# Kernel tuning notes

Hardware: AMD Instinct MI355X
Metric: run time of the kernel (lower is better)

## Reference

```python
import jax, jax.numpy as jnp
import numpy as np

F = 39          # total fields = 13 numeric + 26 categorical
NUM_NUM = 13
N_CAT = 26
V = 100000      # vocab per categorical field
E = 16          # embed size
RED = max(1, F // 3)  # SE reduction size = 13
P = F * (F - 1) // 2  # 741 pairs
HID = [1024, 512, 256]
B = 4096

I_IDX, J_IDX = np.triu_indices(F, k=1)  # static pair indices, len P


def setup_inputs() -> dict:
    key = jax.random.key(0)
    ks = jax.random.split(key, 16)
    s = 0.01
    inp = {
        "cat": jax.random.randint(ks[0], (B, N_CAT), 0, V),
        "num": jax.random.normal(ks[1], (B, NUM_NUM), dtype=jnp.float32),
        "embed_tables": jax.random.normal(ks[2], (N_CAT, V, E), dtype=jnp.float32) * s,
        "num_emb": jax.random.normal(ks[3], (NUM_NUM, E), dtype=jnp.float32) * s,
        "W_se1": jax.random.normal(ks[4], (F, RED), dtype=jnp.float32) * 0.1,
        "W_se2": jax.random.normal(ks[5], (RED, F), dtype=jnp.float32) * 0.1,
        "W_bil": jax.random.normal(ks[6], (F, E, E), dtype=jnp.float32) * 0.1,  # per-field Linear(E,E,no bias), [field,in,out]
        "W_d1": jax.random.normal(ks[7], (2 * P * E, HID[0]), dtype=jnp.float32) * 0.01,
        "b_d1": jnp.zeros((HID[0],), dtype=jnp.float32),
        "W_d2": jax.random.normal(ks[8], (HID[0], HID[1]), dtype=jnp.float32) * 0.02,
        "b_d2": jnp.zeros((HID[1],), dtype=jnp.float32),
        "W_d3": jax.random.normal(ks[9], (HID[1], HID[2]), dtype=jnp.float32) * 0.02,
        "b_d3": jnp.zeros((HID[2],), dtype=jnp.float32),
        "W_out": jax.random.normal(ks[10], (HID[2], 1), dtype=jnp.float32) * 0.02,
        "b_out": jnp.zeros((1,), dtype=jnp.float32),
    }
    return inp


def _bilinear_each(x, W_bil):
    # x: [B,F,E]; project each field with its own matrix, then pairwise multiply.
    proj = jnp.einsum("bfe,fed->bfd", x, W_bil)            # [B,F,E]
    return proj[:, I_IDX, :] * x[:, J_IDX, :]               # [B,P,E]


def reference(cat, num, embed_tables, num_emb, W_se1, W_se2, W_bil,
              W_d1, b_d1, W_d2, b_d2, W_d3, b_d3, W_out, b_out):
    # categorical embeddings: per-field gather -> [B, N_CAT, E]
    cat_embed = embed_tables[jnp.arange(N_CAT)[None, :], cat]
    # numerical "embeddings": value * learned vector -> [B, NUM_NUM, E]
    num_embed = num[:, :, None] * num_emb[None, :, :]
    x = jnp.concatenate([num_embed, cat_embed], axis=1)     # [B,F,E]

    # SENET gating
    Z = jnp.mean(x, axis=-1)                                 # [B,F]
    A = jax.nn.relu(jax.nn.relu(Z @ W_se1) @ W_se2)          # [B,F]
    V = x * A[:, :, None]

    se_bi = _bilinear_each(V, W_bil)                         # [B,P,E]
    bi = _bilinear_each(x, W_bil)                            # [B,P,E]
    hid = jnp.concatenate([se_bi, bi], axis=1).reshape(x.shape[0], -1)  # [B, 2*P*E]

    h = jax.nn.relu(hid @ W_d1 + b_d1)
    h = jax.nn.relu(h @ W_d2 + b_d2)
    h = jax.nn.relu(h @ W_d3 + b_d3)
    return h @ W_out + b_out                                 # [B,1]
```

## Files before the change

kernel.cpp:

```cpp
#include <hip/hip_runtime.h>

typedef unsigned short u16;
typedef __attribute__((ext_vector_type(8))) __bf16 bf16x8;
typedef __attribute__((ext_vector_type(4))) float f32x4;

#define NF    39
#define NNUM  13
#define NCAT  26
#define VOC   100000
#define NPAIR 741
#define KHID  23712
#define BATCH 4096
#define HD1   1024
#define HD2   512
#define HD3   256

__device__ __forceinline__ u16 f2bf(float f) {
  unsigned u = __builtin_bit_cast(unsigned, f);
  return (u16)((u + 0x7fffu + ((u >> 16) & 1u)) >> 16);
}

__device__ __forceinline__ void gload16(const void* g, void* l) {
  __builtin_amdgcn_global_load_lds((const __attribute__((address_space(1))) void*)g,
                                   (__attribute__((address_space(3))) void*)l, 16, 0, 0);
}

__global__ __launch_bounds__(256) void fuse_front(
    const int* __restrict__ cat, const float* __restrict__ num,
    const float* __restrict__ tables, const float* __restrict__ nemb,
    const float* __restrict__ Wse1, const float* __restrict__ Wse2,
    const float* __restrict__ Wbil, u16* __restrict__ hid)
{
  __shared__ float xs[NF][16];
  __shared__ float wb[NF][16][16];
  __shared__ float pr[NF][16];
  __shared__ float Zs[NF], Ts[NNUM], As[NF];
  __shared__ unsigned char pis[NPAIR], pjs[NPAIR];

  const int b = blockIdx.x;
  const int tid = threadIdx.x;

  for (int i = tid; i < NF * 256; i += 256) ((float*)wb)[i] = Wbil[i];

  for (int t = tid; t < NNUM * 16; t += 256) {
    int f = t >> 4, e = t & 15;
    xs[f][e] = num[b * NNUM + f] * nemb[t];
  }
  for (int t = tid; t < NCAT * 16; t += 256) {
    int c = t >> 4, e = t & 15;
    int cv = cat[b * NCAT + c];
    xs[NNUM + c][e] = tables[((size_t)c * VOC + cv) * 16 + e];
  }
  for (int p = tid; p < NPAIR; p += 256) {
    int i = 0, rs = 0;
    while (p >= rs + (NF - 1 - i)) { rs += NF - 1 - i; ++i; }
    pis[p] = (unsigned char)i;
    pjs[p] = (unsigned char)(i + 1 + (p - rs));
  }
  __syncthreads();

  if (tid < NF) {
    float s = 0.f;
    #pragma unroll
    for (int e = 0; e < 16; ++e) s += xs[tid][e];
    Zs[tid] = s * (1.f / 16.f);
  }
  __syncthreads();
  if (tid < NNUM) {
    float s = 0.f;
    for (int f = 0; f < NF; ++f) s += Zs[f] * Wse1[f * NNUM + tid];
    Ts[tid] = fmaxf(s, 0.f);
  }
  __syncthreads();
  if (tid < NF) {
    float s = 0.f;
    for (int r = 0; r < NNUM; ++r) s += Ts[r] * Wse2[r * NF + tid];
    As[tid] = fmaxf(s, 0.f);
  }
  for (int t = tid; t < NF * 16; t += 256) {
    int f = t >> 4, d = t & 15;
    float s = 0.f;
    #pragma unroll
    for (int e = 0; e < 16; ++e) s += xs[f][e] * wb[f][e][d];
    pr[f][d] = s;
  }
  __syncthreads();

  u16* hr = hid + (size_t)b * KHID;
  for (int idx = tid; idx < NPAIR * 16; idx += 256) {
    int p = idx >> 4, e = idx & 15;
    int i = pis[p], j = pjs[p];
    float bv = pr[i][e] * xs[j][e];
    hr[NPAIR * 16 + idx] = f2bf(bv);
    hr[idx] = f2bf(As[i] * As[j] * bv);
  }
}

__global__ __launch_bounds__(256) void transpose_cast(
    const float* __restrict__ in, u16* __restrict__ out, int K, int N)
{
  __shared__ float t[32][33];
  const int k0 = blockIdx.x * 32, n0 = blockIdx.y * 32;
  const int c = threadIdx.x & 31, r = threadIdx.x >> 5;
  #pragma unroll
  for (int it = 0; it < 4; ++it)
    t[r + it * 8][c] = in[(size_t)(k0 + r + it * 8) * N + n0 + c];
  __syncthreads();
  #pragma unroll
  for (int it = 0; it < 4; ++it)
    out[(size_t)(n0 + r + it * 8) * K + k0 + c] = f2bf(t[c][r + it * 8]);
}

__global__ __launch_bounds__(512, 2) void gemm8_bf16(
    const u16* __restrict__ A, const u16* __restrict__ Bt,
    float* __restrict__ Cp, int M, int N, int K, int totku, int kpb)
{
  __shared__ __align__(16) u16 lds[4 * 16384];

  const int tid = threadIdx.x;
  const int wid = tid >> 6, lane = tid & 63;

  const int d = blockIdx.x;
  const int x = d & 7;
  const int j = d >> 3;
  const int mb = ((x & 3) << 2) | (j & 3);
  const int nb = (j >> 2) & 3;
  const int sb = ((x >> 2) << 1) | (j >> 4);

  const int ks0 = sb * kpb;
  const int kunits = (totku - ks0 < kpb) ? (totku - ks0) : kpb;

  const int wm = wid >> 2, wn = wid & 3;
  const int lrow = lane & 15, c0 = lane >> 4;

  const int rA = tid >> 2;
  const int csrc = (tid & 3) ^ ((rA >> 1) & 3);
  const u16* pA = A  + (size_t)((size_t)mb * 256 + rA) * K + (size_t)ks0 * 32 + csrc * 8;
  const u16* pB = Bt + (size_t)((size_t)nb * 256 + rA) * K + (size_t)ks0 * 32 + csrc * 8;
  const size_t rowskip = (size_t)128 * K;
  u16* dA = lds + wid * 512;
  u16* dB = lds + 8192 + wid * 512;

  int offA[8], offB[4];
  #pragma unroll
  for (int m = 0; m < 8; ++m) {
    int r = wm * 128 + m * 16 + lrow;
    offA[m] = r * 32 + ((c0 ^ ((r >> 1) & 3)) << 3);
  }
  #pragma unroll
  for (int n = 0; n < 4; ++n) {
    int r = wn * 64 + n * 16 + lrow;
    offB[n] = 8192 + r * 32 + ((c0 ^ ((r >> 1) & 3)) << 3);
  }

  f32x4 acc[8][4];
  #pragma unroll
  for (int m = 0; m < 8; ++m)
    #pragma unroll
    for (int n = 0; n < 4; ++n) acc[m][n] = f32x4{0.f, 0.f, 0.f, 0.f};

  #pragma unroll
  for (int u = 0; u < 3; ++u) {
    const u16* a = pA + u * 32;
    const u16* b = pB + u * 32;
    u16* da = dA + u * 16384;
    u16* db = dB + u * 16384;
    gload16(a, da);            gload16(a + rowskip, da + 4096);
    gload16(b, db);            gload16(b + rowskip, db + 4096);
  }

  for (int t = 0; t < kunits; ++t) {
    asm volatile("s_waitcnt vmcnt(8)" ::: "memory");
    __builtin_amdgcn_s_barrier();
    __builtin_amdgcn_sched_barrier(0);

    {
      int su = (t + 3 < kunits) ? (t + 3) : (kunits - 1);
      const u16* a = pA + (size_t)su * 32;
      const u16* b = pB + (size_t)su * 32;
      int so = ((t + 3) & 3) * 16384;
      u16* da = dA + so;
      u16* db = dB + so;
      gload16(a, da);          gload16(a + rowskip, da + 4096);
      gload16(b, db);          gload16(b + rowskip, db + 4096);
    }

    const u16* sl = lds + (t & 3) * 16384;
    bf16x8 af[8], bg[4];
    #pragma unroll
    for (int m = 0; m < 8; ++m) af[m] = *reinterpret_cast<const bf16x8*>(sl + offA[m]);
    #pragma unroll
    for (int n = 0; n < 4; ++n) bg[n] = *reinterpret_cast<const bf16x8*>(sl + offB[n]);

    __builtin_amdgcn_s_setprio(1);
    #pragma unroll
    for (int m = 0; m < 8; ++m)
      #pragma unroll
      for (int n = 0; n < 4; ++n)
        acc[m][n] = __builtin_amdgcn_mfma_f32_16x16x32_bf16(af[m], bg[n], acc[m][n], 0, 0, 0);
    __builtin_amdgcn_s_setprio(0);

    __builtin_amdgcn_sched_barrier(0);
  }

  float* C = Cp + (size_t)sb * M * N;
  #pragma unroll
  for (int m = 0; m < 8; ++m) {
    const int rb = mb * 256 + wm * 128 + m * 16 + (lane >> 4) * 4;
    #pragma unroll
    for (int n = 0; n < 4; ++n) {
      const int col = nb * 256 + wn * 64 + n * 16 + (lane & 15);
      #pragma unroll
      for (int j2 = 0; j2 < 4; ++j2)
        __builtin_nontemporal_store(acc[m][n][j2], &C[(size_t)(rb + j2) * N + col]);
    }
  }
}

__global__ __launch_bounds__(256) void gemm_bf16(
    const u16* __restrict__ A, const u16* __restrict__ Bt,
    float* __restrict__ Cp, int M, int N, int K, int kps)
{
  __shared__ __align__(16) u16 lA[128 * 32];
  __shared__ __align__(16) u16 lB[128 * 32];
  const int tid = threadIdx.x;
  const int mb = blockIdx.x, nb = blockIdx.y, sb = blockIdx.z;
  const int w = tid >> 6, lane = tid & 63;
  const int wr = (w >> 1) * 64, wc = (w & 1) * 64;
  const int lrow = lane & 15, lko = (lane >> 4) * 8;

  f32x4 acc[4][4];
  #pragma unroll
  for (int m = 0; m < 4; ++m)
    #pragma unroll
    for (int n = 0; n < 4; ++n) acc[m][n] = f32x4{0.f, 0.f, 0.f, 0.f};

  const u16* Ab = A + (size_t)mb * 128 * K;
  const u16* Bb = Bt + (size_t)nb * 128 * K;
  const int r0 = tid >> 2, inn = (tid & 3) * 8;
  const int l0 = (tid & ~63) * 8, l1 = ((256 + tid) & ~63) * 8;

  const int ks1 = (sb + 1) * kps;
  for (int ks = sb * kps; ks < ks1; ++ks) {
    const int k0 = ks * 32;
    __syncthreads();
    gload16(Ab + (size_t)r0 * K + k0 + inn,        lA + l0);
    gload16(Ab + (size_t)(r0 + 64) * K + k0 + inn, lA + l1);
    gload16(Bb + (size_t)r0 * K + k0 + inn,        lB + l0);
    gload16(Bb + (size_t)(r0 + 64) * K + k0 + inn, lB + l1);
    __syncthreads();
    bf16x8 af[4], bg[4];
    #pragma unroll
    for (int m = 0; m < 4; ++m)
      af[m] = *reinterpret_cast<const bf16x8*>(&lA[(wr + m * 16 + lrow) * 32 + lko]);
    #pragma unroll
    for (int n = 0; n < 4; ++n)
      bg[n] = *reinterpret_cast<const bf16x8*>(&lB[(wc + n * 16 + lrow) * 32 + lko]);
    #pragma unroll
    for (int m = 0; m < 4; ++m)
      #pragma unroll
      for (int n = 0; n < 4; ++n)
        acc[m][n] = __builtin_amdgcn_mfma_f32_16x16x32_bf16(af[m], bg[n], acc[m][n], 0, 0, 0);
  }

  float* C = Cp + (size_t)sb * M * N;
  #pragma unroll
  for (int m = 0; m < 4; ++m) {
    const int rb = mb * 128 + wr + m * 16 + (lane >> 4) * 4;
    #pragma unroll
    for (int n = 0; n < 4; ++n) {
      const int col = nb * 128 + wc + n * 16 + (lane & 15);
      #pragma unroll
      for (int j = 0; j < 4; ++j)
        __builtin_nontemporal_store(acc[m][n][j], &C[(size_t)(rb + j) * N + col]);
    }
  }
}

__global__ __launch_bounds__(256) void reduce_bias_relu_bf16(
    const float* __restrict__ part, int S, size_t MN,
    const float* __restrict__ bias, int nmask, u16* __restrict__ out)
{
  for (size_t i = blockIdx.x * 256ull + threadIdx.x; i < MN; i += (size_t)gridDim.x * 256) {
    float s = 0.f;
    for (int k = 0; k < S; ++k) s += __builtin_nontemporal_load(&part[(size_t)k * MN + i]);
    s += bias[i & nmask];
    out[i] = f2bf(fmaxf(s, 0.f));
  }
}

__global__ __launch_bounds__(256) void reduce_bias_relu_f32(
    const float* __restrict__ part, int S, size_t MN,
    const float* __restrict__ bias, int nmask, float* __restrict__ out)
{
  for (size_t i = blockIdx.x * 256ull + threadIdx.x; i < MN; i += (size_t)gridDim.x * 256) {
    float s = 0.f;
    for (int k = 0; k < S; ++k) s += __builtin_nontemporal_load(&part[(size_t)k * MN + i]);
    s += bias[i & nmask];
    out[i] = fmaxf(s, 0.f);
  }
}

__global__ __launch_bounds__(256) void final_dot(
    const float* __restrict__ h3, const float* __restrict__ Wout,
    const float* __restrict__ bout, float* __restrict__ out)
{
  const int row = blockIdx.x * 4 + (threadIdx.x >> 6);
  const int lane = threadIdx.x & 63;
  const float* hr = h3 + (size_t)row * HD3;
  float s = 0.f;
  #pragma unroll
  for (int i = 0; i < 4; ++i) s += hr[lane + i * 64] * Wout[lane + i * 64];
  #pragma unroll
  for (int off = 32; off; off >>= 1) s += __shfl_down(s, off, 64);
  if (lane == 0) out[row] = s + bout[0];
}

extern "C" void kernel_launch(void* const* d_in, const int* in_sizes, int n_in,
                              void* d_out, int out_size, void* d_ws, size_t ws_size,
                              hipStream_t stream)
{
  const int*   cat    = (const int*)  d_in[0];
  const float* num    = (const float*)d_in[1];
  const float* tables = (const float*)d_in[2];
  const float* nemb   = (const float*)d_in[3];
  const float* Wse1   = (const float*)d_in[4];
  const float* Wse2   = (const float*)d_in[5];
  const float* Wbil   = (const float*)d_in[6];
  const float* Wd1    = (const float*)d_in[7];
  const float* bd1    = (const float*)d_in[8];
  const float* Wd2    = (const float*)d_in[9];
  const float* bd2    = (const float*)d_in[10];
  const float* Wd3    = (const float*)d_in[11];
  const float* bd3    = (const float*)d_in[12];
  const float* Wout   = (const float*)d_in[13];
  const float* bout   = (const float*)d_in[14];

  char* ws = (char*)d_ws;
  u16*   hid  = (u16*)  (ws + 0ull);
  u16*   W1t  = (u16*)  (ws + 194248704ull);
  float* part = (float*)(ws + 242810880ull);
  u16*   W2t  = (u16*)  (ws + 309919744ull);
  u16*   W3t  = (u16*)  (ws + 310968320ull);
  u16*   h1b  = (u16*)  (ws + 0ull);
  u16*   h2b  = (u16*)  (ws + 8388608ull);
  float* h3f  = (float*)(ws + 12582912ull);

  transpose_cast<<<dim3(KHID / 32, HD1 / 32), 256, 0, stream>>>(Wd1, W1t, KHID, HD1);
  transpose_cast<<<dim3(HD1 / 32, HD2 / 32), 256, 0, stream>>>(Wd2, W2t, HD1, HD2);
  transpose_cast<<<dim3(HD2 / 32, HD3 / 32), 256, 0, stream>>>(Wd3, W3t, HD2, HD3);
  fuse_front<<<BATCH, 256, 0, stream>>>(cat, num, tables, nemb, Wse1, Wse2, Wbil, hid);

  gemm8_bf16<<<256, 512, 0, stream>>>(hid, W1t, part, BATCH, HD1, KHID, 741, 186);
  reduce_bias_relu_bf16<<<2048, 256, 0, stream>>>(part, 4, (size_t)BATCH * HD1, bd1, HD1 - 1, h1b);

  gemm_bf16<<<dim3(BATCH / 128, HD2 / 128, 2), 256, 0, stream>>>(h1b, W2t, part, BATCH, HD2, HD1, 16);
  reduce_bias_relu_bf16<<<2048, 256, 0, stream>>>(part, 2, (size_t)BATCH * HD2, bd2, HD2 - 1, h2b);

  gemm_bf16<<<dim3(BATCH / 128, HD3 / 128, 4), 256, 0, stream>>>(h2b, W3t, part, BATCH, HD3, HD2, 4);
  reduce_bias_relu_f32<<<2048, 256, 0, stream>>>(part, 4, (size_t)BATCH * HD3, bd3, HD3 - 1, h3f);

  final_dot<<<BATCH / 4, 256, 0, stream>>>(h3f, Wout, bout, (float*)d_out);
}
```

Before: 381.5 us.

## Restructure big GEMM main loop into ping-pong half-tile phases with staggered loads

The first dense-layer GEMM now splits each K unit into two half-phases of 16 MFMAs. Each phase interleaves LDS fragment reads and global-to-LDS prefetches for A and B separately. A and B get their own 4-slot ring buffers, and the loop is unrolled by two K units, with a tail step for an odd count. The aim is to overlap LDS reads, async global loads and MFMA work better and to hold fewer A fragments in registers, at the cost of more barriers per iteration and tricky vmcnt accounting.

After: 365.0 us. 1.05x faster.

```diff
diff --git a/kernel.cpp b/kernel.cpp
--- a/kernel.cpp
+++ b/kernel.cpp
@@ -111,35 +111,33 @@
     out[(size_t)(n0 + r + it * 8) * K + k0 + c] = f2bf(t[c][r + it * 8]);
 }
 
-__global__ __launch_bounds__(512, 2) void gemm8_bf16(
+__global__ __launch_bounds__(512, 2) void gemm8p_bf16(
     const u16* __restrict__ A, const u16* __restrict__ Bt,
     float* __restrict__ Cp, int M, int N, int K, int totku, int kpb)
 {
-  __shared__ __align__(16) u16 lds[4 * 16384];
+  __shared__ __align__(16) u16 lds[65536];
 
   const int tid = threadIdx.x;
   const int wid = tid >> 6, lane = tid & 63;
 
   const int d = blockIdx.x;
-  const int x = d & 7;
-  const int j = d >> 3;
-  const int mb = ((x & 3) << 2) | (j & 3);
-  const int nb = (j >> 2) & 3;
-  const int sb = ((x >> 2) << 1) | (j >> 4);
+  const int x = d & 7, jj = d >> 3;
+  const int mb = ((x & 3) << 2) | (jj & 3);
+  const int nb = (jj >> 2) & 3;
+  const int sb = ((x >> 2) << 1) | (jj >> 4);
 
   const int ks0 = sb * kpb;
   const int kunits = (totku - ks0 < kpb) ? (totku - ks0) : kpb;
+  const int ftiles = kunits >> 1;
 
   const int wm = wid >> 2, wn = wid & 3;
   const int lrow = lane & 15, c0 = lane >> 4;
 
-  const int rA = tid >> 2;
-  const int csrc = (tid & 3) ^ ((rA >> 1) & 3);
-  const u16* pA = A  + (size_t)((size_t)mb * 256 + rA) * K + (size_t)ks0 * 32 + csrc * 8;
-  const u16* pB = Bt + (size_t)((size_t)nb * 256 + rA) * K + (size_t)ks0 * 32 + csrc * 8;
-  const size_t rowskip = (size_t)128 * K;
-  u16* dA = lds + wid * 512;
-  u16* dB = lds + 8192 + wid * 512;
+  const int rr = tid >> 2, cc = tid & 3, csrc = cc ^ ((rr >> 1) & 3);
+  const u16* pAg = A  + (size_t)((size_t)mb * 256 + rr) * K + (size_t)ks0 * 32 + csrc * 8;
+  const u16* pBg = Bt + (size_t)((size_t)nb * 256 + rr) * K + (size_t)ks0 * 32 + csrc * 8;
+  const size_t rsk = (size_t)128 * K;
+  const int dstoff = tid * 8;
 
   int offA[8], offB[4];
   #pragma unroll
@@ -150,8 +148,17 @@
   #pragma unroll
   for (int n = 0; n < 4; ++n) {
     int r = wn * 64 + n * 16 + lrow;
-    offB[n] = 8192 + r * 32 + ((c0 ^ ((r >> 1) & 3)) << 3);
-  }
+    offB[n] = r * 32 + ((c0 ^ ((r >> 1) & 3)) << 3);
+  }
+
+#define STAGE_A(g) { int sg = ((g) < kunits) ? (g) : (kunits - 1);          \
+    const u16* s_ = pAg + (size_t)sg * 32;                                   \
+    u16* dp_ = lds + (((g) & 3) * 8192) + dstoff;                            \
+    gload16(s_, dp_); gload16(s_ + rsk, dp_ + 4096); }
+#define STAGE_B(g) { int sg = ((g) < kunits) ? (g) : (kunits - 1);          \
+    const u16* s_ = pBg + (size_t)sg * 32;                                   \
+    u16* dp_ = lds + 32768 + (((g) & 3) * 8192) + dstoff;                    \
+    gload16(s_, dp_); gload16(s_ + rsk, dp_ + 4096); }
 
   f32x4 acc[8][4];
   #pragma unroll
@@ -159,49 +166,171 @@
     #pragma unroll
     for (int n = 0; n < 4; ++n) acc[m][n] = f32x4{0.f, 0.f, 0.f, 0.f};
 
-  #pragma unroll
-  for (int u = 0; u < 3; ++u) {
-    const u16* a = pA + u * 32;
-    const u16* b = pB + u * 32;
-    u16* da = dA + u * 16384;
-    u16* db = dB + u * 16384;
-    gload16(a, da);            gload16(a + rowskip, da + 4096);
-    gload16(b, db);            gload16(b + rowskip, db + 4096);
-  }
-
-  for (int t = 0; t < kunits; ++t) {
+  STAGE_A(0); STAGE_B(0); STAGE_A(1); STAGE_B(1); STAGE_A(2); STAGE_B(2); STAGE_B(3);
+  asm volatile("s_waitcnt vmcnt(10)" ::: "memory");
+  __builtin_amdgcn_s_barrier();
+
+  bf16x8 a0, a1, a2, a3, bg0, bg1, bg2, bg3;
+
+  for (int tt = 0; tt < ftiles; ++tt) {
+    const int g0 = tt << 1;
+    const u16* As0 = lds + ((g0 & 3) * 8192);
+    const u16* As1 = lds + (((g0 + 1) & 3) * 8192);
+    const u16* Bs0 = lds + 32768 + ((g0 & 3) * 8192);
+    const u16* Bs1 = lds + 32768 + (((g0 + 1) & 3) * 8192);
+
+    a0 = *reinterpret_cast<const bf16x8*>(As0 + offA[0]);
+    a1 = *reinterpret_cast<const bf16x8*>(As0 + offA[1]);
+    a2 = *reinterpret_cast<const bf16x8*>(As0 + offA[2]);
+    a3 = *reinterpret_cast<const bf16x8*>(As0 + offA[3]);
+    bg0 = *reinterpret_cast<const bf16x8*>(Bs0 + offB[0]);
+    bg1 = *reinterpret_cast<const bf16x8*>(Bs0 + offB[1]);
+    bg2 = *reinterpret_cast<const bf16x8*>(Bs0 + offB[2]);
+    bg3 = *reinterpret_cast<const bf16x8*>(Bs0 + offB[3]);
+    STAGE_A(g0 + 3);
+    __builtin_amdgcn_sched_barrier(0);
+    __builtin_amdgcn_s_barrier();
+    asm volatile("s_waitcnt lgkmcnt(0)" ::: "memory");
+    __builtin_amdgcn_sched_barrier(0);
+    __builtin_amdgcn_s_setprio(1);
+    acc[0][0] = __builtin_amdgcn_mfma_f32_16x16x32_bf16(a0, bg0, acc[0][0], 0, 0, 0);
+    acc[0][1] = __builtin_amdgcn_mfma_f32_16x16x32_bf16(a0, bg1, acc[0][1], 0, 0, 0);
+    acc[0][2] = __builtin_amdgcn_mfma_f32_16x16x32_bf16(a0, bg2, acc[0][2], 0, 0, 0);
+    acc[0][3] = __builtin_amdgcn_mfma_f32_16x16x32_bf16(a0, bg3, acc[0][3], 0, 0, 0);
+    acc[1][0] = __builtin_amdgcn_mfma_f32_16x16x32_bf16(a1, bg0, acc[1][0], 0, 0, 0);
+    acc[1][1] = __builtin_amdgcn_mfma_f32_16x16x32_bf16(a1, bg1, acc[1][1], 0, 0, 0);
+    acc[1][2] = __builtin_amdgcn_mfma_f32_16x16x32_bf16(a1, bg2, acc[1][2], 0, 0, 0);
+    acc[1][3] = __builtin_amdgcn_mfma_f32_16x16x32_bf16(a1, bg3, acc[1][3], 0, 0, 0);
+    acc[2][0] = __builtin_amdgcn_mfma_f32_16x16x32_bf16(a2, bg0, acc[2][0], 0, 0, 0);
+    acc[2][1] = __builtin_amdgcn_mfma_f32_16x16x32_bf16(a2, bg1, acc[2][1], 0, 0, 0);
+    acc[2][2] = __builtin_amdgcn_mfma_f32_16x16x32_bf16(a2, bg2, acc[2][2], 0, 0, 0);
+    acc[2][3] = __builtin_amdgcn_mfma_f32_16x16x32_bf16(a2, bg3, acc[2][3], 0, 0, 0);
+    acc[3][0] = __builtin_amdgcn_mfma_f32_16x16x32_bf16(a3, bg0, acc[3][0], 0, 0, 0);
+    acc[3][1] = __builtin_amdgcn_mfma_f32_16x16x32_bf16(a3, bg1, acc[3][1], 0, 0, 0);
+    acc[3][2] = __builtin_amdgcn_mfma_f32_16x16x32_bf16(a3, bg2, acc[3][2], 0, 0, 0);
+    acc[3][3] = __builtin_amdgcn_mfma_f32_16x16x32_bf16(a3, bg3, acc[3][3], 0, 0, 0);
+    __builtin_amdgcn_s_setprio(0);
+    __builtin_amdgcn_sched_barrier(0);
+    __builtin_amdgcn_s_barrier();
+
+    a0 = *reinterpret_cast<const bf16x8*>(As0 + offA[4]);
+    a1 = *reinterpret_cast<const bf16x8*>(As0 + offA[5]);
+    a2 = *reinterpret_cast<const bf16x8*>(As0 + offA[6]);
+    a3 = *reinterpret_cast<const bf16x8*>(As0 + offA[7]);
+    STAGE_B(g0 + 4);
+    __builtin_amdgcn_sched_barrier(0);
+    __builtin_amdgcn_s_barrier();
+    asm volatile("s_waitcnt lgkmcnt(0)" ::: "memory");
+    __builtin_amdgcn_sched_barrier(0);
+    __builtin_amdgcn_s_setprio(1);
+    acc[4][0] = __builtin_amdgcn_mfma_f32_16x16x32_bf16(a0, bg0, acc[4][0], 0, 0, 0);
+    acc[4][1] = __builtin_amdgcn_mfma_f32_16x16x32_bf16(a0, bg1, acc[4][1], 0, 0, 0);
+    acc[4][2] = __builtin_amdgcn_mfma_f32_16x16x32_bf16(a0, bg2, acc[4][2], 0, 0, 0);
+    acc[4][3] = __builtin_amdgcn_mfma_f32_16x16x32_bf16(a0, bg3, acc[4][3], 0, 0, 0);
+    acc[5][0] = __builtin_amdgcn_mfma_f32_16x16x32_bf16(a1, bg0, acc[5][0], 0, 0, 0);
+    acc[5][1] = __builtin_amdgcn_mfma_f32_16x16x32_bf16(a1, bg1, acc[5][1], 0, 0, 0);
+    acc[5][2] = __builtin_amdgcn_mfma_f32_16x16x32_bf16(a1, bg2, acc[5][2], 0, 0, 0);
+    acc[5][3] = __builtin_amdgcn_mfma_f32_16x16x32_bf16(a1, bg3, acc[5][3], 0, 0, 0);
+    acc[6][0] = __builtin_amdgcn_mfma_f32_16x16x32_bf16(a2, bg0, acc[6][0], 0, 0, 0);
+    acc[6][1] = __builtin_amdgcn_mfma_f32_16x16x32_bf16(a2, bg1, acc[6][1], 0, 0, 0);
+    acc[6][2] = __builtin_amdgcn_mfma_f32_16x16x32_bf16(a2, bg2, acc[6][2], 0, 0, 0);
+    acc[6][3] = __builtin_amdgcn_mfma_f32_16x16x32_bf16(a2, bg3, acc[6][3], 0, 0, 0);
+    acc[7][0] = __builtin_amdgcn_mfma_f32_16x16x32_bf16(a3, bg0, acc[7][0], 0, 0, 0);
+    acc[7][1] = __builtin_amdgcn_mfma_f32_16x16x32_bf16(a3, bg1, acc[7][1], 0, 0, 0);
+    acc[7][2] = __builtin_amdgcn_mfma_f32_16x16x32_bf16(a3, bg2, acc[7][2], 0, 0, 0);
+    acc[7][3] = __builtin_amdgcn_mfma_f32_16x16x32_bf16(a3, bg3, acc[7][3], 0, 0, 0);
+    __builtin_amdgcn_s_setprio(0);
+    __builtin_amdgcn_sched_barrier(0);
     asm volatile("s_waitcnt vmcnt(8)" ::: "memory");
     __builtin_amdgcn_s_barrier();
-    __builtin_amdgcn_sched_barrier(0);
-
-    {
-      int su = (t + 3 < kunits) ? (t + 3) : (kunits - 1);
-      const u16* a = pA + (size_t)su * 32;
-      const u16* b = pB + (size_t)su * 32;
-      int so = ((t + 3) & 3) * 16384;
-      u16* da = dA + so;
-      u16* db = dB + so;
-      gload16(a, da);          gload16(a + rowskip, da + 4096);
-      gload16(b, db);          gload16(b + rowskip, db + 4096);
+
+    a0 = *reinterpret_cast<const bf16x8*>(As1 + offA[0]);
+    a1 = *reinterpret_cast<const bf16x8*>(As1 + offA[1]);
+    a2 = *reinterpret_cast<const bf16x8*>(As1 + offA[2]);
+    a3 = *reinterpret_cast<const bf16x8*>(As1 + offA[3]);
+    bg0 = *reinterpret_cast<const bf16x8*>(Bs1 + offB[0]);
+    bg1 = *reinterpret_cast<const bf16x8*>(Bs1 + offB[1]);
+    bg2 = *reinterpret_cast<const bf16x8*>(Bs1 + offB[2]);
+    bg3 = *reinterpret_cast<const bf16x8*>(Bs1 + offB[3]);
+    STAGE_A(g0 + 4);
+    __builtin_amdgcn_sched_barrier(0);
+    __builtin_amdgcn_s_barrier();
+    asm volatile("s_waitcnt lgkmcnt(0)" ::: "memory");
+    __builtin_amdgcn_sched_barrier(0);
+    __builtin_amdgcn_s_setprio(1);
+    acc[0][0] = __builtin_amdgcn_mfma_f32_16x16x32_bf16(a0, bg0, acc[0][0], 0, 0, 0);
+    acc[0][1] = __builtin_amdgcn_mfma_f32_16x16x32_bf16(a0, bg1, acc[0][1], 0, 0, 0);
+    acc[0][2] = __builtin_amdgcn_mfma_f32_16x16x32_bf16(a0, bg2, acc[0][2], 0, 0, 0);
+    acc[0][3] = __builtin_amdgcn_mfma_f32_16x16x32_bf16(a0, bg3, acc[0][3], 0, 0, 0);
+    acc[1][0] = __builtin_amdgcn_mfma_f32_16x16x32_bf16(a1, bg0, acc[1][0], 0, 0, 0);
+    acc[1][1] = __builtin_amdgcn_mfma_f32_16x16x32_bf16(a1, bg1, acc[1][1], 0, 0, 0);
+    acc[1][2] = __builtin_amdgcn_mfma_f32_16x16x32_bf16(a1, bg2, acc[1][2], 0, 0, 0);
+    acc[1][3] = __builtin_amdgcn_mfma_f32_16x16x32_bf16(a1, bg3, acc[1][3], 0, 0, 0);
+    acc[2][0] = __builtin_amdgcn_mfma_f32_16x16x32_bf16(a2, bg0, acc[2][0], 0, 0, 0);
+    acc[2][1] = __builtin_amdgcn_mfma_f32_16x16x32_bf16(a2, bg1, acc[2][1], 0, 0, 0);
+    acc[2][2] = __builtin_amdgcn_mfma_f32_16x16x32_bf16(a2, bg2, acc[2][2], 0, 0, 0);
+    acc[2][3] = __builtin_amdgcn_mfma_f32_16x16x32_bf16(a2, bg3, acc[2][3], 0, 0, 0);
+    acc[3][0] = __builtin_amdgcn_mfma_f32_16x16x32_bf16(a3, bg0, acc[3][0], 0, 0, 0);
+    acc[3][1] = __builtin_amdgcn_mfma_f32_16x16x32_bf16(a3, bg1, acc[3][1], 0, 0, 0);
+    acc[3][2] = __builtin_amdgcn_mfma_f32_16x16x32_bf16(a3, bg2, acc[3][2], 0, 0, 0);
+    acc[3][3] = __builtin_amdgcn_mfma_f32_16x16x32_bf16(a3, bg3, acc[3][3], 0, 0, 0);
+    __builtin_amdgcn_s_setprio(0);
+    __builtin_amdgcn_sched_barrier(0);
+    __builtin_amdgcn_s_barrier();
+
+    a0 = *reinterpret_cast<const bf16x8*>(As1 + offA[4]);
+    a1 = *reinterpret_cast<const bf16x8*>(As1 + offA[5]);
+    a2 = *reinterpret_cast<const bf16x8*>(As1 + offA[6]);
+    a3 = *reinterpret_cast<const bf16x8*>(As1 + offA[7]);
+    STAGE_B(g0 + 5);
+    __builtin_amdgcn_sched_barrier(0);
+    __builtin_amdgcn_s_barrier();
+    asm volatile("s_waitcnt lgkmcnt(0)" ::: "memory");
+    __builtin_amdgcn_sched_barrier(0);
+    __builtin_amdgcn_s_setprio(1);
+    acc[4][0] = __builtin_amdgcn_mfma_f32_16x16x32_bf16(a0, bg0, acc[4][0], 0, 0, 0);
+    acc[4][1] = __builtin_amdgcn_mfma_f32_16x16x32_bf16(a0, bg1, acc[4][1], 0, 0, 0);
+    acc[4][2] = __builtin_amdgcn_mfma_f32_16x16x32_bf16(a0, bg2, acc[4][2], 0, 0, 0);
+    acc[4][3] = __builtin_amdgcn_mfma_f32_16x16x32_bf16(a0, bg3, acc[4][3], 0, 0, 0);
+    acc[5][0] = __builtin_amdgcn_mfma_f32_16x16x32_bf16(a1, bg0, acc[5][0], 0, 0, 0);
+    acc[5][1] = __builtin_amdgcn_mfma_f32_16x16x32_bf16(a1, bg1, acc[5][1], 0, 0, 0);
+    acc[5][2] = __builtin_amdgcn_mfma_f32_16x16x32_bf16(a1, bg2, acc[5][2], 0, 0, 0);
+    acc[5][3] = __builtin_amdgcn_mfma_f32_16x16x32_bf16(a1, bg3, acc[5][3], 0, 0, 0);
+    acc[6][0] = __builtin_amdgcn_mfma_f32_16x16x32_bf16(a2, bg0, acc[6][0], 0, 0, 0);
+    acc[6][1] = __builtin_amdgcn_mfma_f32_16x16x32_bf16(a2, bg1, acc[6][1], 0, 0, 0);
+    acc[6][2] = __builtin_amdgcn_mfma_f32_16x16x32_bf16(a2, bg2, acc[6][2], 0, 0, 0);
+    acc[6][3] = __builtin_amdgcn_mfma_f32_16x16x32_bf16(a2, bg3, acc[6][3], 0, 0, 0);
+    acc[7][0] = __builtin_amdgcn_mfma_f32_16x16x32_bf16(a3, bg0, acc[7][0], 0, 0, 0);
+    acc[7][1] = __builtin_amdgcn_mfma_f32_16x16x32_bf16(a3, bg1, acc[7][1], 0, 0, 0);
+    acc[7][2] = __builtin_amdgcn_mfma_f32_16x16x32_bf16(a3, bg2, acc[7][2], 0, 0, 0);
+    acc[7][3] = __builtin_amdgcn_mfma_f32_16x16x32_bf16(a3, bg3, acc[7][3], 0, 0, 0);
+    __builtin_amdgcn_s_setprio(0);
+    __builtin_amdgcn_sched_barrier(0);
+    asm volatile("s_waitcnt vmcnt(8)" ::: "memory");
+    __builtin_amdgcn_s_barrier();
+  }
+
+  if (kunits & 1) {
+    asm volatile("s_waitcnt vmcnt(0)" ::: "memory");
+    __builtin_amdgcn_s_barrier();
+    const int g = kunits - 1;
+    const u16* As = lds + ((g & 3) * 8192);
+    const u16* Bs = lds + 32768 + ((g & 3) * 8192);
+    bg0 = *reinterpret_cast<const bf16x8*>(Bs + offB[0]);
+    bg1 = *reinterpret_cast<const bf16x8*>(Bs + offB[1]);
+    bg2 = *reinterpret_cast<const bf16x8*>(Bs + offB[2]);
+    bg3 = *reinterpret_cast<const bf16x8*>(Bs + offB[3]);
+    #pragma unroll
+    for (int m = 0; m < 8; ++m) {
+      bf16x8 am = *reinterpret_cast<const bf16x8*>(As + offA[m]);
+      acc[m][0] = __builtin_amdgcn_mfma_f32_16x16x32_bf16(am, bg0, acc[m][0], 0, 0, 0);
+      acc[m][1] = __builtin_amdgcn_mfma_f32_16x16x32_bf16(am, bg1, acc[m][1], 0, 0, 0);
+      acc[m][2] = __builtin_amdgcn_mfma_f32_16x16x32_bf16(am, bg2, acc[m][2], 0, 0, 0);
+      acc[m][3] = __builtin_amdgcn_mfma_f32_16x16x32_bf16(am, bg3, acc[m][3], 0, 0, 0);
     }
-
-    const u16* sl = lds + (t & 3) * 16384;
-    bf16x8 af[8], bg[4];
-    #pragma unroll
-    for (int m = 0; m < 8; ++m) af[m] = *reinterpret_cast<const bf16x8*>(sl + offA[m]);
-    #pragma unroll
-    for (int n = 0; n < 4; ++n) bg[n] = *reinterpret_cast<const bf16x8*>(sl + offB[n]);
-
-    __builtin_amdgcn_s_setprio(1);
-    #pragma unroll
-    for (int m = 0; m < 8; ++m)
-      #pragma unroll
-      for (int n = 0; n < 4; ++n)
-        acc[m][n] = __builtin_amdgcn_mfma_f32_16x16x32_bf16(af[m], bg[n], acc[m][n], 0, 0, 0);
-    __builtin_amdgcn_s_setprio(0);
-
-    __builtin_amdgcn_sched_barrier(0);
-  }
+  }
+#undef STAGE_A
+#undef STAGE_B
 
   float* C = Cp + (size_t)sb * M * N;
   #pragma unroll
@@ -351,7 +480,7 @@
   transpose_cast<<<dim3(HD2 / 32, HD3 / 32), 256, 0, stream>>>(Wd3, W3t, HD2, HD3);
   fuse_front<<<BATCH, 256, 0, stream>>>(cat, num, tables, nemb, Wse1, Wse2, Wbil, hid);
 
-  gemm8_bf16<<<256, 512, 0, stream>>>(hid, W1t, part, BATCH, HD1, KHID, 741, 186);
+  gemm8p_bf16<<<256, 512, 0, stream>>>(hid, W1t, part, BATCH, HD1, KHID, 741, 186);
   reduce_bias_relu_bf16<<<2048, 256, 0, stream>>>(part, 4, (size_t)BATCH * HD1, bd1, HD1 - 1, h1b);
 
   gemm_bf16<<<dim3(BATCH / 128, HD2 / 128, 2), 256, 0, stream>>>(h1b, W2t, part, BATCH, HD2, HD1, 16);
```
